# Performance work log

Measured on AMD Instinct MI355X. Metric: run time of the kernel, lower is better.

## Reference

```python
import jax, jax.numpy as jnp
import numpy as np

B, T, D, H = 16, 2048, 128, 4  # batch, seq_len, dim (fixed=128 in source), nheads (fixed=4)


def setup_inputs() -> dict:
    key = jax.random.key(0)
    k1, k2, k3 = jax.random.split(key, 3)
    x = jax.random.normal(k1, (B, T, D), dtype=jnp.float32)
    # nn.Linear(dim, 3*dim, bias=False): y = x @ W^T; we store W^T directly as [in, out]
    w_attn = jax.random.normal(k2, (D, 3 * D), dtype=jnp.float32) * 0.05
    w_proj = jax.random.normal(k3, (D, D), dtype=jnp.float32) * 0.05
    return {"x": x, "w_attn": w_attn, "w_proj": w_proj}


def reference(x, w_attn, w_proj):
    Bb, Tt, Dd = x.shape
    Dh = Dd // H  # head_size = 32
    # fused QKV projection
    qkv = x @ w_attn                       # [B, T, 3D]
    q, k, v = jnp.split(qkv, 3, axis=-1)   # each [B, T, D]

    def to_heads(t):
        return t.reshape(Bb, Tt, H, Dh).transpose(0, 2, 1, 3)  # [B, H, T, Dh]

    q, k, v = to_heads(q), to_heads(k), to_heads(v)
    scale = 1.0 / jnp.sqrt(jnp.float32(Dh))
    scores = jnp.einsum('bhqd,bhkd->bhqk', q, k) * scale       # [B, H, T, T]
    causal = jnp.tril(jnp.ones((Tt, Tt), dtype=bool))
    scores = jnp.where(causal, scores, jnp.finfo(scores.dtype).min)
    attn = jax.nn.softmax(scores, axis=-1)
    y = jnp.einsum('bhqk,bhkd->bhqd', attn, v)                 # [B, H, T, Dh]
    y = y.transpose(0, 2, 1, 3).reshape(Bb, Tt, Dd)            # [B, T, D]
    # output projection (resid dropout is identity in eval mode)
    return y @ w_proj
```

## Files before the change

kernel.cpp:

```cpp
#include <hip/hip_runtime.h>
#include <math.h>

typedef __attribute__((ext_vector_type(8))) short short8;
typedef __attribute__((ext_vector_type(4))) short short4v;
typedef __attribute__((ext_vector_type(4))) float f32x4;
typedef __attribute__((ext_vector_type(16))) float f32x16;
typedef unsigned int u32;
typedef unsigned short u16;

#define Bsz 16
#define Tsz 2048
#define Dsz 128
#define Msz (Bsz*Tsz)

#define QSCALE_LOG2 0.2550348715f

#if __has_builtin(__builtin_amdgcn_exp2f)
#define EXP2(x) __builtin_amdgcn_exp2f(x)
#else
#define EXP2(x) exp2f(x)
#endif

__device__ __forceinline__ u16 f2bf(float f) {
    union { float f; unsigned int u; } v; v.f = f;
    unsigned int u = v.u;
    return (u16)((u + 0x7FFFu + ((u >> 16) & 1u)) >> 16);
}

__device__ __forceinline__ u32 cvtpk(float lo, float hi) {
    u32 r; asm("v_cvt_pk_bf16_f32 %0, %1, %2" : "=v"(r) : "v"(lo), "v"(hi)); return r;
}
__device__ __forceinline__ void swap32u(u32 &a, u32 &b) {
    asm("v_permlane32_swap_b32 %0, %1" : "+v"(a), "+v"(b));
}


__global__ __launch_bounds__(256) void transpose_both_kernel(const float* __restrict__ wa,
                                                             const float* __restrict__ wp,
                                                             u16* __restrict__ wT,
                                                             u16* __restrict__ wpT) {
    int idx = blockIdx.x * 256 + threadIdx.x;
    if (idx < 384 * 128) {
        int n = idx >> 7, k = idx & 127;
        wT[idx] = f2bf(wa[(size_t)k * 384 + n]);
    } else {
        int i = idx - 384 * 128;
        int n = i >> 7, k = i & 127;
        wpT[i] = f2bf(wp[(size_t)k * 128 + n]);
    }
}

template<bool QKV>
__global__ __launch_bounds__(128) void gemm_mfma_kernel(const void* __restrict__ Ap,
                                                        const u16* __restrict__ WT,
                                                        float* __restrict__ out,
                                                        u16* __restrict__ qPk,
                                                        u16* __restrict__ kPk,
                                                        u16* __restrict__ vPk) {
    const int w = threadIdx.x >> 6, l = threadIdx.x & 63;
    const int lg = l >> 4, lc = l & 15;
    const int row0 = blockIdx.x * 16;

    short8 a[4];
    if (QKV) {
        const float* xr = (const float*)Ap + (size_t)(row0 + lc) * 128;
        #pragma unroll
        for (int kk = 0; kk < 4; ++kk) {
            const float4* xp = (const float4*)(xr + kk * 32 + lg * 8);
            float4 u0 = xp[0], u1 = xp[1];
            u16 t8[8] = {f2bf(u0.x), f2bf(u0.y), f2bf(u0.z), f2bf(u0.w),
                         f2bf(u1.x), f2bf(u1.y), f2bf(u1.z), f2bf(u1.w)};
            a[kk] = *(short8*)t8;
        }
    } else {
        const u16* ar = (const u16*)Ap + (size_t)(row0 + lc) * 128;
        #pragma unroll
        for (int kk = 0; kk < 4; ++kk)
            a[kk] = *(const short8*)(ar + kk * 32 + lg * 8);
    }

    const int NCT = QKV ? 3 : 1;
    #pragma unroll
    for (int i = 0; i < NCT; ++i) {
        const int col0 = (w + 2 * i) * 64;
        const bool vtile = QKV && col0 >= 256;
        f32x4 acc[4];
        #pragma unroll
        for (int j = 0; j < 4; ++j) acc[j] = (f32x4){0.f, 0.f, 0.f, 0.f};

        #pragma unroll
        for (int j = 0; j < 4; ++j) {
            const u16* wp = WT + (size_t)(col0 + j * 16 + lc) * 128;
            #pragma unroll
            for (int kk = 0; kk < 4; ++kk) {
                short8 bw = *(const short8*)(wp + kk * 32 + lg * 8);
                if (vtile)
                    acc[j] = __builtin_amdgcn_mfma_f32_16x16x32_bf16(a[kk], bw, acc[j], 0, 0, 0);
                else
                    acc[j] = __builtin_amdgcn_mfma_f32_16x16x32_bf16(bw, a[kk], acc[j], 0, 0, 0);
            }
        }

        if (!QKV) {
            #pragma unroll
            for (int j = 0; j < 4; ++j) {
                int c0 = col0 + j * 16 + lg * 4;
                *(f32x4*)(out + (size_t)(row0 + lc) * 128 + c0) = acc[j];
            }
        } else if (vtile) {
            #pragma unroll
            for (int j = 0; j < 4; ++j) {
                int cv = col0 + j * 16 + lc - 256;
                int hh = cv >> 5, dh = cv & 31;
                int grow = row0 + lg * 4;
                int bb = grow >> 11, t0 = grow & 2047;
                int bh = bb * 4 + hh;
                int g = t0 >> 5, tp = t0 & 31;
                int f = tp >> 4, hi2 = (tp & 15) >> 3, j0 = tp & 7;
                u16 o4[4];
                #pragma unroll
                for (int r = 0; r < 4; ++r) o4[r] = f2bf(acc[j][r]);
                *(short4v*)(vPk + ((size_t)((bh * 64 + g) * 2 + f)) * 512
                                 + (hi2 * 32 + dh) * 8 + j0) = *(short4v*)o4;
            }
        } else {
            u16* dst = (col0 < 128) ? qPk : kPk;
            const float sc = (col0 < 128) ? QSCALE_LOG2 : 1.0f;
            const int t = row0 + lc;
            const int bb = t >> 11, tt = t & 2047;
            const int g = tt >> 5, lq = tt & 31;
            #pragma unroll
            for (int j = 0; j < 4; ++j) {
                int c0 = (col0 + j * 16 + lg * 4) & 127;
                int hh = c0 >> 5, dh0 = c0 & 31;
                int bh = bb * 4 + hh;
                int f = dh0 >> 4, hi2 = (dh0 & 15) >> 3, j0 = dh0 & 7;
                u16 o4[4];
                #pragma unroll
                for (int r = 0; r < 4; ++r) o4[r] = f2bf(acc[j][r] * sc);
                *(short4v*)(dst + ((size_t)((bh * 64 + g) * 2 + f)) * 512
                                 + (hi2 * 32 + lq) * 8 + j0) = *(short4v*)o4;
            }
        }
    }
}

__global__ __launch_bounds__(256) void attn_fixed_kernel(const u16* __restrict__ qPk,
                                                         const u16* __restrict__ kPk,
                                                         const u16* __restrict__ vPk,
                                                         u16* __restrict__ y) {
    const int w = threadIdx.x >> 6, l = threadIdx.x & 63;
    const int bh = blockIdx.x, b = bh >> 2, h = bh & 3;
    const int iq = 63 - (int)blockIdx.y;
    const int q0 = iq * 32;
    const int lq = l & 31, hi = l >> 5;

    __shared__ float Ll[4][32];
    __shared__ float Osc[4][32][32];

    const u16* qp = qPk + ((size_t)(bh * 64 + iq) * 2) * 512 + l * 8;
    const short8 qf0 = *(const short8*)(qp);
    const short8 qf1 = *(const short8*)(qp + 512);

    const u16* kbase = kPk + (size_t)bh * 64 * 1024 + l * 8;
    const u16* vbase = vPk + (size_t)bh * 64 * 1024 + l * 8;

    const float z0 = (float)((int)blockDim.x >> 16);
    f32x16 zc;
    #pragma unroll
    for (int r = 0; r < 16; ++r) zc[r] = z0;

    f32x16 o;
    #pragma unroll
    for (int r = 0; r < 16; ++r) o[r] = 0.f;
    float lsum = 0.f;

    auto process = [&](short8 ka, short8 kb, short8 va, short8 vb, bool diag) {
        f32x16 s;
        __builtin_amdgcn_s_setprio(1);
        s = __builtin_amdgcn_mfma_f32_32x32x16_bf16(ka, qf0, zc, 0, 0, 0);
        s = __builtin_amdgcn_mfma_f32_32x32x16_bf16(kb, qf1, s, 0, 0, 0);
        __builtin_amdgcn_s_setprio(0);

        if (diag) {
            #pragma unroll
            for (int r = 0; r < 16; ++r) {
                int crow = (r & 3) + 8 * (r >> 2) + 4 * hi;
                if (crow > lq) s[r] = -INFINITY;
            }
        }

        float p[16];
        #pragma unroll
        for (int r = 0; r < 16; ++r) p[r] = EXP2(s[r]);

        float ts[8];
        #pragma unroll
        for (int j = 0; j < 8; ++j) ts[j] = p[2 * j] + p[2 * j + 1];
        #pragma unroll
        for (int j = 0; j < 4; ++j) ts[j] = ts[j] + ts[j + 4];
        lsum += (ts[0] + ts[2]) + (ts[1] + ts[3]);

        u32 a0 = cvtpk(p[0], p[1]),   a1 = cvtpk(p[2], p[3]);
        u32 b0 = cvtpk(p[4], p[5]),   b1 = cvtpk(p[6], p[7]);
        swap32u(a0, b0); swap32u(a1, b1);
        u32 c0 = cvtpk(p[8], p[9]),   c1 = cvtpk(p[10], p[11]);
        u32 d0 = cvtpk(p[12], p[13]), d1 = cvtpk(p[14], p[15]);
        swap32u(c0, d0); swap32u(c1, d1);
        u32 pa0[4] = {a0, a1, b0, b1};
        u32 pa1[4] = {c0, c1, d0, d1};
        __builtin_amdgcn_s_setprio(1);
        o = __builtin_amdgcn_mfma_f32_32x32x16_bf16(*(short8*)pa0, va, o, 0, 0, 0);
        o = __builtin_amdgcn_mfma_f32_32x32x16_bf16(*(short8*)pa1, vb, o, 0, 0, 0);
        __builtin_amdgcn_s_setprio(0);
    };

    if (w <= iq) {
        int g = w;
        const u16* kp = kbase + (size_t)g * 1024;
        const u16* vp = vbase + (size_t)g * 1024;
        short8 kf0 = *(const short8*)kp, kf1 = *(const short8*)(kp + 512);
        short8 vf0 = *(const short8*)vp, vf1 = *(const short8*)(vp + 512);
        #pragma unroll 2
        while (g + 4 <= iq) {
            const u16* kp2 = kbase + (size_t)(g + 4) * 1024;
            const u16* vp2 = vbase + (size_t)(g + 4) * 1024;
            short8 nk0 = *(const short8*)kp2, nk1 = *(const short8*)(kp2 + 512);
            short8 nv0 = *(const short8*)vp2, nv1 = *(const short8*)(vp2 + 512);
            process(kf0, kf1, vf0, vf1, false);
            kf0 = nk0; kf1 = nk1; vf0 = nv0; vf1 = nv1;
            g += 4;
        }
        process(kf0, kf1, vf0, vf1, g == iq);
    }

    lsum += __shfl_xor(lsum, 32, 64);
    if (hi == 0) Ll[w][lq] = lsum;
    #pragma unroll
    for (int r = 0; r < 16; ++r) {
        int crow = (r & 3) + 8 * (r >> 2) + 4 * hi;
        Osc[w][crow][lq] = o[r];
    }
    __syncthreads();

    const int p0 = (int)threadIdx.x * 4;
    const int qq = p0 >> 5, dh0 = p0 & 31;
    float Lt = (Ll[0][qq] + Ll[1][qq]) + (Ll[2][qq] + Ll[3][qq]);
    float invL = 1.0f / Lt;
    f32x4 s0 = *(const f32x4*)&Osc[0][qq][dh0];
    f32x4 s1 = *(const f32x4*)&Osc[1][qq][dh0];
    f32x4 s2 = *(const f32x4*)&Osc[2][qq][dh0];
    f32x4 s3 = *(const f32x4*)&Osc[3][qq][dh0];
    u16 ov[4];
    #pragma unroll
    for (int j = 0; j < 4; ++j)
        ov[j] = f2bf(((s0[j] + s1[j]) + (s2[j] + s3[j])) * invL);
    *(short4v*)(y + ((size_t)b * Tsz + q0 + qq) * 128 + h * 32 + dh0) = *(short4v*)ov;
}

extern "C" void kernel_launch(void* const* d_in, const int* in_sizes, int n_in,
                              void* d_out, int out_size, void* d_ws, size_t ws_size,
                              hipStream_t stream) {
    const float* x      = (const float*)d_in[0];
    const float* w_attn = (const float*)d_in[1];
    const float* w_proj = (const float*)d_in[2];
    float* out = (float*)d_out;

    char* ws = (char*)d_ws;
    u16* qPk  = (u16*)(ws);
    u16* kPk  = (u16*)(ws + ((size_t)8  << 20));
    u16* vPk  = (u16*)(ws + ((size_t)16 << 20));
    u16* y_bf = (u16*)(ws + ((size_t)24 << 20));
    u16* wT   = (u16*)(ws + ((size_t)32 << 20));
    u16* wpT  = (u16*)(ws + ((size_t)33 << 20));

    transpose_both_kernel<<<(512 * 128) / 256, 256, 0, stream>>>(w_attn, w_proj, wT, wpT);

    gemm_mfma_kernel<true><<<dim3(Msz / 16), 128, 0, stream>>>(x, wT, nullptr, qPk, kPk, vPk);

    attn_fixed_kernel<<<dim3(Bsz * 4, 64), 256, 0, stream>>>(qPk, kPk, vPk, y_bf);

    gemm_mfma_kernel<false><<<dim3(Msz / 16), 128, 0, stream>>>(y_bf, wpT, out, nullptr, nullptr, nullptr);
}
```

Before: 87.57 us.

## Fuse all four stages into one cooperative persistent kernel with grid syncs

Replaces the four separate launches (weight transpose, QKV GEMM, attention, output GEMM) with a single cooperative kernel of 512 persistent blocks that separates the stages with grid.sync(). The attention stage is reorganised so each job covers four query tiles (63-by, 47-by, 16+by, by), pairing long and short causal rows to balance work across blocks. This removes per-launch overhead and tail gaps between stages. In exchange it adds grid-wide barriers, and the 512-block grid with a 2-blocks-per-CU bound limits occupancy compared with the original 4096-block attention grid. It falls back to the old launches if the cooperative launch fails.

Measured after the change: 246.3 us. +181.2%, slower.

```diff
diff --git a/kernel.cpp b/kernel.cpp
--- a/kernel.cpp
+++ b/kernel.cpp
@@ -1,5 +1,8 @@
 #include <hip/hip_runtime.h>
+#include <hip/hip_cooperative_groups.h>
 #include <math.h>
+
+namespace cg = cooperative_groups;
 
 typedef __attribute__((ext_vector_type(8))) short short8;
 typedef __attribute__((ext_vector_type(4))) short short4v;
@@ -32,6 +35,259 @@
 }
 __device__ __forceinline__ void swap32u(u32 &a, u32 &b) {
     asm("v_permlane32_swap_b32 %0, %1" : "+v"(a), "+v"(b));
+}
+
+
+__global__ __launch_bounds__(256, 2) void fused_csa_kernel(
+        const float* __restrict__ x,  const float* __restrict__ wa,
+        const float* __restrict__ wp, float* __restrict__ out,
+        u16* __restrict__ qPk, u16* __restrict__ kPk, u16* __restrict__ vPk,
+        u16* __restrict__ y,   u16* __restrict__ wT,  u16* __restrict__ wpT) {
+    cg::grid_group grid = cg::this_grid();
+    const int tid = threadIdx.x;
+    const int w = tid >> 6, l = tid & 63;
+    const int lg = l >> 4, lc = l & 15;
+    const int nblk = (int)gridDim.x;
+
+    __shared__ float Ll[4][32];
+    __shared__ float Osc[4][32][32];
+
+    for (int idx = (int)blockIdx.x * 256 + tid; idx < 512 * 128; idx += nblk * 256) {
+        if (idx < 384 * 128) {
+            int n = idx >> 7, k = idx & 127;
+            wT[idx] = f2bf(wa[(size_t)k * 384 + n]);
+        } else {
+            int i = idx - 384 * 128;
+            int n = i >> 7, k = i & 127;
+            wpT[i] = f2bf(wp[(size_t)k * 128 + n]);
+        }
+    }
+    grid.sync();
+
+    for (int gw = (int)blockIdx.x * 4 + w; gw < 4096; gw += nblk * 4) {
+        const int row0 = (gw >> 1) * 16;
+        const int wl = gw & 1;
+
+        short8 a[4];
+        const float* xr = x + (size_t)(row0 + lc) * 128;
+        #pragma unroll
+        for (int kk = 0; kk < 4; ++kk) {
+            const float4* xp = (const float4*)(xr + kk * 32 + lg * 8);
+            float4 u0 = xp[0], u1 = xp[1];
+            u16 t8[8] = {f2bf(u0.x), f2bf(u0.y), f2bf(u0.z), f2bf(u0.w),
+                         f2bf(u1.x), f2bf(u1.y), f2bf(u1.z), f2bf(u1.w)};
+            a[kk] = *(short8*)t8;
+        }
+
+        #pragma unroll
+        for (int i = 0; i < 3; ++i) {
+            const int col0 = (wl + 2 * i) * 64;
+            const bool vtile = col0 >= 256;
+            f32x4 acc[4];
+            #pragma unroll
+            for (int j = 0; j < 4; ++j) acc[j] = (f32x4){0.f, 0.f, 0.f, 0.f};
+
+            #pragma unroll
+            for (int j = 0; j < 4; ++j) {
+                const u16* wpr = wT + (size_t)(col0 + j * 16 + lc) * 128;
+                #pragma unroll
+                for (int kk = 0; kk < 4; ++kk) {
+                    short8 bw = *(const short8*)(wpr + kk * 32 + lg * 8);
+                    if (vtile)
+                        acc[j] = __builtin_amdgcn_mfma_f32_16x16x32_bf16(a[kk], bw, acc[j], 0, 0, 0);
+                    else
+                        acc[j] = __builtin_amdgcn_mfma_f32_16x16x32_bf16(bw, a[kk], acc[j], 0, 0, 0);
+                }
+            }
+
+            if (vtile) {
+                #pragma unroll
+                for (int j = 0; j < 4; ++j) {
+                    int cv = col0 + j * 16 + lc - 256;
+                    int hh = cv >> 5, dh = cv & 31;
+                    int grow = row0 + lg * 4;
+                    int bb = grow >> 11, t0 = grow & 2047;
+                    int bh = bb * 4 + hh;
+                    int g = t0 >> 5, tp = t0 & 31;
+                    int f = tp >> 4, hi2 = (tp & 15) >> 3, j0 = tp & 7;
+                    u16 o4[4];
+                    #pragma unroll
+                    for (int r = 0; r < 4; ++r) o4[r] = f2bf(acc[j][r]);
+                    *(short4v*)(vPk + ((size_t)((bh * 64 + g) * 2 + f)) * 512
+                                     + (hi2 * 32 + dh) * 8 + j0) = *(short4v*)o4;
+                }
+            } else {
+                u16* dst = (col0 < 128) ? qPk : kPk;
+                const float sc = (col0 < 128) ? QSCALE_LOG2 : 1.0f;
+                const int t = row0 + lc;
+                const int bb = t >> 11, tt = t & 2047;
+                const int g = tt >> 5, lq2 = tt & 31;
+                #pragma unroll
+                for (int j = 0; j < 4; ++j) {
+                    int c0 = (col0 + j * 16 + lg * 4) & 127;
+                    int hh = c0 >> 5, dh0 = c0 & 31;
+                    int bh = bb * 4 + hh;
+                    int f = dh0 >> 4, hi2 = (dh0 & 15) >> 3, j0 = dh0 & 7;
+                    u16 o4[4];
+                    #pragma unroll
+                    for (int r = 0; r < 4; ++r) o4[r] = f2bf(acc[j][r] * sc);
+                    *(short4v*)(dst + ((size_t)((bh * 64 + g) * 2 + f)) * 512
+                                     + (hi2 * 32 + lq2) * 8 + j0) = *(short4v*)o4;
+                }
+            }
+        }
+    }
+    grid.sync();
+
+    {
+        const int lq = l & 31, hi = l >> 5;
+        const float z0 = (float)((int)blockDim.x >> 16);
+        f32x16 zc;
+        #pragma unroll
+        for (int r = 0; r < 16; ++r) zc[r] = z0;
+
+        for (int job = (int)blockIdx.x; job < 1024; job += nblk) {
+            const int bh = job & 63, by = job >> 6;
+            const int b = bh >> 2, h = bh & 3;
+
+            const u16* kbase = kPk + (size_t)bh * 65536 + l * 8;
+            const u16* vbase = vPk + (size_t)bh * 65536 + l * 8;
+
+            const int jobs[4] = {63 - by, 47 - by, 16 + by, by};
+
+            #pragma unroll 1
+            for (int ji = 0; ji < 4; ++ji) {
+                const int iq = jobs[ji];
+                const int q0 = iq * 32;
+
+                const u16* qp = qPk + ((size_t)(bh * 64 + iq) * 2) * 512 + l * 8;
+                const short8 qf0 = *(const short8*)(qp);
+                const short8 qf1 = *(const short8*)(qp + 512);
+
+                f32x16 o;
+                #pragma unroll
+                for (int r = 0; r < 16; ++r) o[r] = 0.f;
+                float lsum = 0.f;
+
+                auto process = [&](short8 ka, short8 kb, short8 va, short8 vb, bool diag) {
+                    f32x16 s;
+                    __builtin_amdgcn_s_setprio(1);
+                    s = __builtin_amdgcn_mfma_f32_32x32x16_bf16(ka, qf0, zc, 0, 0, 0);
+                    s = __builtin_amdgcn_mfma_f32_32x32x16_bf16(kb, qf1, s, 0, 0, 0);
+                    __builtin_amdgcn_s_setprio(0);
+
+                    if (diag) {
+                        #pragma unroll
+                        for (int r = 0; r < 16; ++r) {
+                            int crow = (r & 3) + 8 * (r >> 2) + 4 * hi;
+                            if (crow > lq) s[r] = -INFINITY;
+                        }
+                    }
+
+                    float p[16];
+                    #pragma unroll
+                    for (int r = 0; r < 16; ++r) p[r] = EXP2(s[r]);
+
+                    float ts[8];
+                    #pragma unroll
+                    for (int j = 0; j < 8; ++j) ts[j] = p[2 * j] + p[2 * j + 1];
+                    #pragma unroll
+                    for (int j = 0; j < 4; ++j) ts[j] = ts[j] + ts[j + 4];
+                    lsum += (ts[0] + ts[2]) + (ts[1] + ts[3]);
+
+                    u32 a0 = cvtpk(p[0], p[1]),   a1 = cvtpk(p[2], p[3]);
+                    u32 b0 = cvtpk(p[4], p[5]),   b1 = cvtpk(p[6], p[7]);
+                    swap32u(a0, b0); swap32u(a1, b1);
+                    u32 c0 = cvtpk(p[8], p[9]),   c1 = cvtpk(p[10], p[11]);
+                    u32 d0 = cvtpk(p[12], p[13]), d1 = cvtpk(p[14], p[15]);
+                    swap32u(c0, d0); swap32u(c1, d1);
+                    u32 pa0[4] = {a0, a1, b0, b1};
+                    u32 pa1[4] = {c0, c1, d0, d1};
+                    __builtin_amdgcn_s_setprio(1);
+                    o = __builtin_amdgcn_mfma_f32_32x32x16_bf16(*(short8*)pa0, va, o, 0, 0, 0);
+                    o = __builtin_amdgcn_mfma_f32_32x32x16_bf16(*(short8*)pa1, vb, o, 0, 0, 0);
+                    __builtin_amdgcn_s_setprio(0);
+                };
+
+                if (w <= iq) {
+                    int g = w;
+                    const u16* kp = kbase + (size_t)g * 1024;
+                    const u16* vp = vbase + (size_t)g * 1024;
+                    short8 kf0 = *(const short8*)kp, kf1 = *(const short8*)(kp + 512);
+                    short8 vf0 = *(const short8*)vp, vf1 = *(const short8*)(vp + 512);
+                    #pragma unroll 2
+                    while (g + 4 <= iq) {
+                        const u16* kp2 = kbase + (size_t)(g + 4) * 1024;
+                        const u16* vp2 = vbase + (size_t)(g + 4) * 1024;
+                        short8 nk0 = *(const short8*)kp2, nk1 = *(const short8*)(kp2 + 512);
+                        short8 nv0 = *(const short8*)vp2, nv1 = *(const short8*)(vp2 + 512);
+                        process(kf0, kf1, vf0, vf1, false);
+                        kf0 = nk0; kf1 = nk1; vf0 = nv0; vf1 = nv1;
+                        g += 4;
+                    }
+                    process(kf0, kf1, vf0, vf1, g == iq);
+                }
+
+                lsum += __shfl_xor(lsum, 32, 64);
+                if (hi == 0) Ll[w][lq] = lsum;
+                #pragma unroll
+                for (int r = 0; r < 16; ++r) {
+                    int crow = (r & 3) + 8 * (r >> 2) + 4 * hi;
+                    Osc[w][crow][lq] = o[r];
+                }
+                __syncthreads();
+
+                const int p0 = tid * 4;
+                const int qq = p0 >> 5, dh0 = p0 & 31;
+                float Lt = (Ll[0][qq] + Ll[1][qq]) + (Ll[2][qq] + Ll[3][qq]);
+                float invL = 1.0f / Lt;
+                f32x4 s0 = *(const f32x4*)&Osc[0][qq][dh0];
+                f32x4 s1 = *(const f32x4*)&Osc[1][qq][dh0];
+                f32x4 s2 = *(const f32x4*)&Osc[2][qq][dh0];
+                f32x4 s3 = *(const f32x4*)&Osc[3][qq][dh0];
+                u16 ov[4];
+                #pragma unroll
+                for (int j = 0; j < 4; ++j)
+                    ov[j] = f2bf(((s0[j] + s1[j]) + (s2[j] + s3[j])) * invL);
+                *(short4v*)(y + ((size_t)b * Tsz + q0 + qq) * 128 + h * 32 + dh0) = *(short4v*)ov;
+
+                __syncthreads();
+            }
+        }
+    }
+    grid.sync();
+
+    for (int gw = (int)blockIdx.x * 4 + w; gw < 4096; gw += nblk * 4) {
+        const int row0 = (gw >> 1) * 16;
+        const int wl = gw & 1;
+
+        short8 a[4];
+        const u16* ar = y + (size_t)(row0 + lc) * 128;
+        #pragma unroll
+        for (int kk = 0; kk < 4; ++kk)
+            a[kk] = *(const short8*)(ar + kk * 32 + lg * 8);
+
+        const int col0 = wl * 64;
+        f32x4 acc[4];
+        #pragma unroll
+        for (int j = 0; j < 4; ++j) acc[j] = (f32x4){0.f, 0.f, 0.f, 0.f};
+
+        #pragma unroll
+        for (int j = 0; j < 4; ++j) {
+            const u16* wpr = wpT + (size_t)(col0 + j * 16 + lc) * 128;
+            #pragma unroll
+            for (int kk = 0; kk < 4; ++kk) {
+                short8 bw = *(const short8*)(wpr + kk * 32 + lg * 8);
+                acc[j] = __builtin_amdgcn_mfma_f32_16x16x32_bf16(bw, a[kk], acc[j], 0, 0, 0);
+            }
+        }
+
+        #pragma unroll
+        for (int j = 0; j < 4; ++j) {
+            int c0 = col0 + j * 16 + lg * 4;
+            *(f32x4*)(out + (size_t)(row0 + lc) * 128 + c0) = acc[j];
+        }
+    }
 }
 
 
@@ -90,10 +346,10 @@
 
         #pragma unroll
         for (int j = 0; j < 4; ++j) {
-            const u16* wp = WT + (size_t)(col0 + j * 16 + lc) * 128;
+            const u16* wpr = WT + (size_t)(col0 + j * 16 + lc) * 128;
             #pragma unroll
             for (int kk = 0; kk < 4; ++kk) {
-                short8 bw = *(const short8*)(wp + kk * 32 + lg * 8);
+                short8 bw = *(const short8*)(wpr + kk * 32 + lg * 8);
                 if (vtile)
                     acc[j] = __builtin_amdgcn_mfma_f32_16x16x32_bf16(a[kk], bw, acc[j], 0, 0, 0);
                 else
@@ -128,7 +384,7 @@
             const float sc = (col0 < 128) ? QSCALE_LOG2 : 1.0f;
             const int t = row0 + lc;
             const int bb = t >> 11, tt = t & 2047;
-            const int g = tt >> 5, lq = tt & 31;
+            const int g = tt >> 5, lq2 = tt & 31;
             #pragma unroll
             for (int j = 0; j < 4; ++j) {
                 int c0 = (col0 + j * 16 + lg * 4) & 127;
@@ -139,7 +395,7 @@
                 #pragma unroll
                 for (int r = 0; r < 4; ++r) o4[r] = f2bf(acc[j][r] * sc);
                 *(short4v*)(dst + ((size_t)((bh * 64 + g) * 2 + f)) * 512
-                                 + (hi2 * 32 + lq) * 8 + j0) = *(short4v*)o4;
+                                 + (hi2 * 32 + lq2) * 8 + j0) = *(short4v*)o4;
             }
         }
     }
@@ -162,8 +418,8 @@
     const short8 qf0 = *(const short8*)(qp);
     const short8 qf1 = *(const short8*)(qp + 512);
 
-    const u16* kbase = kPk + (size_t)bh * 64 * 1024 + l * 8;
-    const u16* vbase = vPk + (size_t)bh * 64 * 1024 + l * 8;
+    const u16* kbase = kPk + (size_t)bh * 65536 + l * 8;
+    const u16* vbase = vPk + (size_t)bh * 65536 + l * 8;
 
     const float z0 = (float)((int)blockDim.x >> 16);
     f32x16 zc;
@@ -274,11 +530,15 @@
     u16* wT   = (u16*)(ws + ((size_t)32 << 20));
     u16* wpT  = (u16*)(ws + ((size_t)33 << 20));
 
-    transpose_both_kernel<<<(512 * 128) / 256, 256, 0, stream>>>(w_attn, w_proj, wT, wpT);
-
-    gemm_mfma_kernel<true><<<dim3(Msz / 16), 128, 0, stream>>>(x, wT, nullptr, qPk, kPk, vPk);
-
-    attn_fixed_kernel<<<dim3(Bsz * 4, 64), 256, 0, stream>>>(qPk, kPk, vPk, y_bf);
-
-    gemm_mfma_kernel<false><<<dim3(Msz / 16), 128, 0, stream>>>(y_bf, wpT, out, nullptr, nullptr, nullptr);
-}
+    void* args[] = {(void*)&x, (void*)&w_attn, (void*)&w_proj, (void*)&out,
+                    (void*)&qPk, (void*)&kPk, (void*)&vPk,
+                    (void*)&y_bf, (void*)&wT, (void*)&wpT};
+    hipError_t err = hipLaunchCooperativeKernel((const void*)fused_csa_kernel,
+                                                dim3(512), dim3(256), args, 0, stream);
+    if (err != hipSuccess) {
+        transpose_both_kernel<<<(512 * 128) / 256, 256, 0, stream>>>(w_attn, w_proj, wT, wpT);
+        gemm_mfma_kernel<true><<<dim3(Msz / 16), 128, 0, stream>>>(x, wT, nullptr, qPk, kPk, vPk);
+        attn_fixed_kernel<<<dim3(Bsz * 4, 64), 256, 0, stream>>>(qPk, kPk, vPk, y_bf);
+        gemm_mfma_kernel<false><<<dim3(Msz / 16), 128, 0, stream>>>(y_bf, wpT, out, nullptr, nullptr, nullptr);
+    }
+}
```
